# Optimization experiments

Hardware: AMD Instinct MI355X
Metric: run time of the kernel (lower is better)

Reference implementation:

```python
import jax, jax.numpy as jnp
import numpy as np

B, N, C, H = 4, 8192, 1024, 16
D = C // H

def setup_inputs() -> dict:
    key = jax.random.key(0)
    k1, k2, k3 = jax.random.split(key, 3)
    scale_in = 1.0 / np.sqrt(C)
    return {
        "x": jax.random.normal(k1, (B, N, C), dtype=jnp.float32),
        "w_qkv": jax.random.normal(k2, (C, 3 * C), dtype=jnp.float32) * scale_in,
        "b_qkv": jnp.zeros((3 * C,), dtype=jnp.float32),
        "w_proj": jax.random.normal(k3, (C, C), dtype=jnp.float32) * scale_in,
        "b_proj": jnp.zeros((C,), dtype=jnp.float32),
    }

def reference(x, w_qkv, b_qkv, w_proj, b_proj):
    Bx, Nx, Cx = x.shape
    qkv = x @ w_qkv + b_qkv                       # [B,N,3C]
    qkv = qkv.reshape(Bx, Nx, 3, H, D)
    qkv = jnp.transpose(qkv, (2, 0, 3, 1, 4))     # [3,B,H,N,D]
    q, k, v = qkv[0], qkv[1], qkv[2]
    q = jax.nn.elu(q) + 1.0                       # positive feature map
    k = jax.nn.elu(k) + 1.0
    kv = jnp.einsum('bhnd,bhne->bhde', k, v)      # [B,H,D,D]
    out = jnp.einsum('bhnd,bhde->bhne', q, kv)    # [B,H,N,D]
    z = 1.0 / (jnp.einsum('bhnd,bhd->bhn', q, k.sum(axis=2)) + 1e-8)
    out = out * z[..., None]
    out = jnp.transpose(out, (0, 2, 1, 3)).reshape(Bx, Nx, Cx)
    out = out @ w_proj + b_proj                   # dropout is identity in eval
    return out
```

## Files before the change

kernel.cpp:

```cpp
#include <hip/hip_runtime.h>
#include <hip/hip_bf16.h>
#include <stdint.h>

typedef unsigned short ushort_t;
typedef __attribute__((ext_vector_type(8))) short short8;
typedef __attribute__((ext_vector_type(4))) short short4v;
typedef __attribute__((ext_vector_type(4))) float floatx4;

__device__ __forceinline__ ushort_t f2b(float f) {
    unsigned u = __float_as_uint(f);
    unsigned r = (u + 0x7FFFu + ((u >> 16) & 1u)) >> 16;
    return (ushort_t)r;
}
__device__ __forceinline__ float b2f(ushort_t h) {
    return __uint_as_float(((unsigned)h) << 16);
}
__device__ __forceinline__ float elu1(float f) {
    return (f > 0.f) ? (f + 1.f) : __expf(f);
}

#define GLDS16(srcp, dstp)                                                          \
    __builtin_amdgcn_global_load_lds(                                               \
        (const __attribute__((address_space(1))) unsigned int*)(srcp),              \
        (__attribute__((address_space(3))) unsigned int*)(dstp), 16, 0, 0)

__device__ __forceinline__ short4v tr16(const ushort_t* p) {
    short4v r;
    const __attribute__((address_space(3))) ushort_t* p3 =
        (const __attribute__((address_space(3))) ushort_t*)p;
    asm volatile("ds_read_b64_tr_b16 %0, %1" : "=v"(r) : "v"(p3));
    return r;
}


__global__ void conv_bf16(const float* __restrict__ in, ushort_t* __restrict__ out, int n8) {
    for (int i = blockIdx.x * blockDim.x + threadIdx.x; i < n8; i += gridDim.x * blockDim.x) {
        const float4 f0 = *(const float4*)&in[(size_t)i * 8];
        const float4 f1 = *(const float4*)&in[(size_t)i * 8 + 4];
        ushort4 o0, o1;
        o0.x = f2b(f0.x); o0.y = f2b(f0.y); o0.z = f2b(f0.z); o0.w = f2b(f0.w);
        o1.x = f2b(f1.x); o1.y = f2b(f1.y); o1.z = f2b(f1.z); o1.w = f2b(f1.w);
        *(ushort4*)&out[(size_t)i * 8]     = o0;
        *(ushort4*)&out[(size_t)i * 8 + 4] = o1;
    }
}

__global__ void transpose_conv(const float* __restrict__ in, ushort_t* __restrict__ out,
                               int R, int C) {
    __shared__ float tile[32][33];
    int c0 = blockIdx.x * 32, r0 = blockIdx.y * 32;
    int tx = threadIdx.x, ty = threadIdx.y;
#pragma unroll
    for (int k = 0; k < 4; ++k) {
        int a = ty * 4 + k;
        tile[a][tx] = in[(size_t)(r0 + a) * C + c0 + tx];
    }
    __syncthreads();
#pragma unroll
    for (int k = 0; k < 4; ++k) {
        int a = ty * 4 + k;
        out[(size_t)(c0 + a) * R + r0 + tx] = f2b(tile[tx][a]);
    }
}

__global__ void zero_f32(float* __restrict__ p, int n) {
    int i = blockIdx.x * blockDim.x + threadIdx.x;
    if (i < n) p[i] = 0.f;
}

template<int MODE>
__global__ __launch_bounds__(512, 2) void gemm256(
    const ushort_t* __restrict__ A, const ushort_t* __restrict__ Bt,
    const float* __restrict__ bias,
    ushort_t* __restrict__ out_u16, float* __restrict__ out_f32,
    int Nt, int nbx, int nt)
{
    extern __shared__ ushort_t lds[];
    constexpr int KK = 1024;

    const int tid  = threadIdx.x;
    const int wave = tid >> 6;
    const int lane = tid & 63;
    const int wm_i = wave >> 2;
    const int wn_i = wave & 3;
    const int fr   = lane & 15;
    const int fq   = lane >> 4;

    const int bid  = (int)blockIdx.x;
    const int bswz = ((bid & 7) << 5) + (bid >> 3);
    const int ntiles = nt << 8;

    const int trow = tid >> 3;
    const int csw  = ((tid & 7) ^ (trow & 7)) << 3;
    const int tcolB = ((tid >> 8) << 6) + (trow & 31);

    const int dstA = wave * 512;
    const int dstB = 16384 + wave * 512;

    const int sw0 = (fq ^ (fr & 7)) << 3;
    const int sw1 = sw0 ^ 32;
    const int abase = (wm_i * 64 + fr) * 64;
    const int bbase = (wn_i * 32 + fr) * 64;
    int loA0[2][2], loA1[2][2], loB0[2][2], loB1[2][2];
#pragma unroll
    for (int bf = 0; bf < 2; ++bf)
#pragma unroll
        for (int q = 0; q < 2; ++q) {
            loA0[bf][q] = bf * 32768 + q * 8192 + abase + sw0;
            loA1[bf][q] = bf * 32768 + q * 8192 + abase + sw1;
            loB0[bf][q] = bf * 32768 + 16384 + q * 8192 + bbase + sw0;
            loB1[bf][q] = bf * 32768 + 16384 + q * 8192 + bbase + sw1;
        }

    floatx4 acc[8][4];
    const floatx4 z4 = {0.f, 0.f, 0.f, 0.f};
#pragma unroll
    for (int i = 0; i < 8; ++i)
#pragma unroll
        for (int j = 0; j < 4; ++j) acc[i][j] = z4;

    short8 a[4][2], b[2][2];

    auto tilebase = [&](int t, const ushort_t*& sA, const ushort_t*& sB, int& mm, int& nn) {
        const int byy = t / nbx;
        const int bxx = t - byy * nbx;
        mm = byy << 8; nn = bxx << 8;
        sA = A  + (size_t)(mm + trow)  * KK + csw;
        sB = Bt + (size_t)(nn + tcolB) * KK + csw;
    };

    auto stageA = [&](const ushort_t* sp, int buf, int h, int ko) {
        ushort_t* d = lds + buf * 32768 + h * 8192 + dstA;
        GLDS16(sp + h * (64 * KK) + ko, d);
        GLDS16(sp + h * (64 * KK) + 128 * KK + ko, d + 4096);
    };
    auto stageB = [&](const ushort_t* sp, int buf, int h, int ko) {
        ushort_t* d = lds + buf * 32768 + h * 8192 + dstB;
        GLDS16(sp + h * (32 * KK) + ko, d);
        GLDS16(sp + h * (32 * KK) + 128 * KK + ko, d + 4096);
    };
    auto loadA = [&](int buf, int qr) {
        const int o0 = loA0[buf][qr], o1 = loA1[buf][qr];
#pragma unroll
        for (int i = 0; i < 4; ++i) {
            a[i][0] = *(const short8*)(lds + o0 + i * 1024);
            a[i][1] = *(const short8*)(lds + o1 + i * 1024);
        }
    };
    auto loadB = [&](int buf, int qc) {
        const int o0 = loB0[buf][qc], o1 = loB1[buf][qc];
#pragma unroll
        for (int j = 0; j < 2; ++j) {
            b[j][0] = *(const short8*)(lds + o0 + j * 1024);
            b[j][1] = *(const short8*)(lds + o1 + j * 1024);
        }
    };
    auto mma = [&](int qr, int qc) {
#pragma unroll
        for (int i = 0; i < 4; ++i)
#pragma unroll
            for (int j = 0; j < 2; ++j) {
                acc[qr * 4 + i][qc * 2 + j] =
                    __builtin_amdgcn_mfma_f32_16x16x32_bf16(b[j][0], a[i][0], acc[qr * 4 + i][qc * 2 + j], 0, 0, 0);
                acc[qr * 4 + i][qc * 2 + j] =
                    __builtin_amdgcn_mfma_f32_16x16x32_bf16(b[j][1], a[i][1], acc[qr * 4 + i][qc * 2 + j], 0, 0, 0);
            }
    };

    auto epilogue = [&](int m0, int n0) {
        float4 bv[4];
#pragma unroll
        for (int cj = 0; cj < 4; ++cj) {
            const int nb = n0 + wn_i * 64 + (cj >> 1) * 32 + (cj & 1) * 16 + fq * 4;
            bv[cj] = *(const float4*)&bias[nb];
        }
#pragma unroll
        for (int ri = 0; ri < 8; ++ri) {
            const int m = m0 + wm_i * 128 + (ri >> 2) * 64 + (ri & 3) * 16 + fr;
#pragma unroll
            for (int cj = 0; cj < 4; ++cj) {
                const int col = n0 + wn_i * 64 + (cj >> 1) * 32 + (cj & 1) * 16 + fq * 4;
                float v0 = acc[ri][cj][0] + bv[cj].x;
                float v1 = acc[ri][cj][1] + bv[cj].y;
                float v2 = acc[ri][cj][2] + bv[cj].z;
                float v3 = acc[ri][cj][3] + bv[cj].w;
                if (MODE == 0) {
                    const int s  = col >> 10;
                    const int c  = col & 1023;
                    const int h  = c >> 6;
                    const int d  = c & 63;
                    const int bb = m >> 13;
                    const int n  = m & 8191;
                    if (s < 2) { v0 = elu1(v0); v1 = elu1(v1); v2 = elu1(v2); v3 = elu1(v3); }
                    ushort4 o;
                    o.x = f2b(v0); o.y = f2b(v1); o.z = f2b(v2); o.w = f2b(v3);
                    *(ushort4*)&out_u16[(((size_t)s * 64 + bb * 16 + h) * 8192 + n) * 64 + d] = o;
                } else {
                    float4 o; o.x = v0; o.y = v1; o.z = v2; o.w = v3;
                    *(float4*)&out_f32[(size_t)m * Nt + col] = o;
                }
            }
        }
    };

#define PRIO1() __builtin_amdgcn_s_setprio(1)
#define BOUT()  __builtin_amdgcn_s_setprio(0); __builtin_amdgcn_s_barrier()
#define VM6()   asm volatile("s_waitcnt vmcnt(6)" ::: "memory")

    const ushort_t *saC, *sbC, *saN, *sbN;
    int m0, n0, m0N, n0N;
    int tC = bswz;
    tilebase(tC, saC, sbC, m0, n0);
    int tN = (tC + 256 < ntiles) ? tC + 256 : tC;
    tilebase(tN, saN, sbN, m0N, n0N);

    stageA(saC, 0, 0, 0);
    stageB(sbC, 0, 1, 0);
    stageA(saC, 0, 1, 0);
    stageB(sbC, 0, 0, 0);
    stageA(saC, 1, 0, 64);
    stageB(sbC, 1, 1, 64);
    stageA(saC, 1, 1, 64);
    VM6();
    __builtin_amdgcn_s_barrier();

    for (int ot = 0; ot < nt; ++ot) {
        int ko = 0;
        for (int pr = 0; pr < 7; ++pr, ko += 128) {
            loadA(0, 0); loadB(0, 0);
            stageB(sbC, 1, 0, ko + 64);
            PRIO1(); mma(0, 0); BOUT();

            loadB(0, 1);
            stageA(saC, 0, 0, ko + 128);
            PRIO1(); mma(0, 1); BOUT();

            loadA(0, 1);
            stageB(sbC, 0, 1, ko + 128);
            PRIO1(); mma(1, 1); BOUT();

            loadB(0, 0);
            stageA(saC, 0, 1, ko + 128);
            PRIO1(); mma(1, 0); __builtin_amdgcn_s_setprio(0); VM6();
            __builtin_amdgcn_s_barrier();

            loadA(1, 0); loadB(1, 0);
            stageB(sbC, 0, 0, ko + 128);
            PRIO1(); mma(0, 0); BOUT();

            loadB(1, 1);
            stageA(saC, 1, 0, ko + 192);
            PRIO1(); mma(0, 1); BOUT();

            loadA(1, 1);
            stageB(sbC, 1, 1, ko + 192);
            PRIO1(); mma(1, 1); BOUT();

            loadB(1, 0);
            stageA(saC, 1, 1, ko + 192);
            PRIO1(); mma(1, 0); __builtin_amdgcn_s_setprio(0); VM6();
            __builtin_amdgcn_s_barrier();
        }

        loadA(0, 0); loadB(0, 0);
        stageB(sbC, 1, 0, 960);
        PRIO1(); mma(0, 0); BOUT();

        loadB(0, 1);
        stageA(saN, 0, 0, 0);
        PRIO1(); mma(0, 1); BOUT();

        loadA(0, 1);
        stageB(sbN, 0, 1, 0);
        PRIO1(); mma(1, 1); BOUT();

        loadB(0, 0);
        stageA(saN, 0, 1, 0);
        PRIO1(); mma(1, 0); __builtin_amdgcn_s_setprio(0); VM6();
        __builtin_amdgcn_s_barrier();

        loadA(1, 0); loadB(1, 0);
        stageB(sbN, 0, 0, 0);
        PRIO1(); mma(0, 0); BOUT();

        loadB(1, 1);
        stageA(saN, 1, 0, 64);
        PRIO1(); mma(0, 1); BOUT();

        loadA(1, 1);
        stageB(sbN, 1, 1, 64);
        PRIO1(); mma(1, 1); BOUT();

        loadB(1, 0);
        stageA(saN, 1, 1, 64);
        PRIO1(); mma(1, 0); __builtin_amdgcn_s_setprio(0); VM6();
        __builtin_amdgcn_s_barrier();

        epilogue(m0, n0);
#pragma unroll
        for (int i = 0; i < 8; ++i)
#pragma unroll
            for (int j = 0; j < 4; ++j) acc[i][j] = z4;

        saC = saN; sbC = sbN; m0 = m0N; n0 = n0N; tC = tN;
        tN = (tC + 256 < ntiles) ? tC + 256 : tC;
        tilebase(tN, saN, sbN, m0N, n0N);
    }

#undef PRIO1
#undef BOUT
#undef VM6
}

__global__ __launch_bounds__(256) void kvg2_kernel(
    const ushort_t* __restrict__ kbuf, const ushort_t* __restrict__ vbuf,
    float* __restrict__ kv, float* __restrict__ ksum)
{
    __shared__ ushort_t stg[4][2][4096] __attribute__((aligned(16)));
    __shared__ float ksr[4][64];

    const int bh = blockIdx.y, chunk = blockIdx.x, t = threadIdx.x;
    const int wave = t >> 6, lane = t & 63;
    const int fr = lane & 15, fq = lane >> 4;

    const int srow = lane >> 3;
    const int dcp  = lane & 7;
    const int woff = (dcp >> 1) * 1024 + srow * 16 + (dcp & 1) * 8;

    const int troff = fq * 256 + fr * 8;

    short8 ones;
#pragma unroll
    for (int i = 0; i < 8; ++i) ones[i] = (short)0x3F80;

    floatx4 av[4][4], ak[4];
    const floatx4 z4 = {0.f, 0.f, 0.f, 0.f};
#pragma unroll
    for (int i = 0; i < 4; ++i) {
        ak[i] = z4;
#pragma unroll
        for (int j = 0; j < 4; ++j) av[i][j] = z4;
    }

    const size_t rowbase = (size_t)bh * 8192;
    ushort_t* kreg = &stg[wave][0][0];
    ushort_t* vreg = &stg[wave][1][0];

#pragma unroll 1
    for (int s2 = 0; s2 < 4; ++s2) {
        const int n0 = chunk * 1024 + wave * 256 + s2 * 64;
#pragma unroll
        for (int g = 0; g < 8; ++g) {
            const int n = g * 8 + srow;
            const size_t src = (rowbase + n0 + n) * 64 + dcp * 8;
            *(short8*)&kreg[woff + g * 128] = *(const short8*)&kbuf[src];
            *(short8*)&vreg[woff + g * 128] = *(const short8*)&vbuf[src];
        }
        asm volatile("s_waitcnt lgkmcnt(0)" ::: "memory");
        __builtin_amdgcn_sched_barrier(0);

#pragma unroll
        for (int ns = 0; ns < 2; ++ns) {
            short8 ka[4], vb[4];
#pragma unroll
            for (int dt = 0; dt < 4; ++dt) {
                const ushort_t* kb = kreg + dt * 1024 + ns * 512;
                short4v lo = tr16((const ushort_t*)((const char*)kb + troff));
                short4v hi = tr16((const ushort_t*)((const char*)kb + troff + 128));
                ka[dt] = __builtin_shufflevector(lo, hi, 0, 1, 2, 3, 4, 5, 6, 7);
            }
#pragma unroll
            for (int et = 0; et < 4; ++et) {
                const ushort_t* vB = vreg + et * 1024 + ns * 512;
                short4v lo = tr16((const ushort_t*)((const char*)vB + troff));
                short4v hi = tr16((const ushort_t*)((const char*)vB + troff + 128));
                vb[et] = __builtin_shufflevector(lo, hi, 0, 1, 2, 3, 4, 5, 6, 7);
            }
            asm volatile("s_waitcnt lgkmcnt(0)" ::: "memory");
            __builtin_amdgcn_sched_barrier(0);

#pragma unroll
            for (int dt = 0; dt < 4; ++dt) {
                ak[dt] = __builtin_amdgcn_mfma_f32_16x16x32_bf16(ka[dt], ones, ak[dt], 0, 0, 0);
#pragma unroll
                for (int et = 0; et < 4; ++et)
                    av[dt][et] = __builtin_amdgcn_mfma_f32_16x16x32_bf16(ka[dt], vb[et], av[dt][et], 0, 0, 0);
            }
        }
    }

    float* red = (float*)&stg[wave][0][0];
#pragma unroll
    for (int dt = 0; dt < 4; ++dt)
#pragma unroll
        for (int et = 0; et < 4; ++et)
#pragma unroll
            for (int r = 0; r < 4; ++r)
                red[(dt * 16 + fq * 4 + r) * 64 + et * 16 + fr] = av[dt][et][r];
    if (fr == 0) {
#pragma unroll
        for (int dt = 0; dt < 4; ++dt)
#pragma unroll
            for (int r = 0; r < 4; ++r)
                ksr[wave][dt * 16 + fq * 4 + r] = ak[dt][r];
    }
    __syncthreads();

    const float* base = (const float*)&stg[0][0][0];
#pragma unroll
    for (int j = 0; j < 4; ++j) {
        const int idx = t * 16 + j * 4;
        float4 s0 = *(const float4*)&base[0 * 4096 + idx];
        float4 s1 = *(const float4*)&base[1 * 4096 + idx];
        float4 s2 = *(const float4*)&base[2 * 4096 + idx];
        float4 s3 = *(const float4*)&base[3 * 4096 + idx];
        atomicAdd(&kv[(size_t)bh * 4096 + idx + 0], s0.x + s1.x + s2.x + s3.x);
        atomicAdd(&kv[(size_t)bh * 4096 + idx + 1], s0.y + s1.y + s2.y + s3.y);
        atomicAdd(&kv[(size_t)bh * 4096 + idx + 2], s0.z + s1.z + s2.z + s3.z);
        atomicAdd(&kv[(size_t)bh * 4096 + idx + 3], s0.w + s1.w + s2.w + s3.w);
    }
    if (t < 64) {
        float s = ksr[0][t] + ksr[1][t] + ksr[2][t] + ksr[3][t];
        atomicAdd(&ksum[bh * 64 + t], s);
    }
}

__global__ __launch_bounds__(256) void out_kernel(
    const ushort_t* __restrict__ qbuf, const float* __restrict__ kv,
    const float* __restrict__ ksum, ushort_t* __restrict__ obuf)
{
    __shared__ float kvs[4096];
    __shared__ float ksums[64];

    const int bh = blockIdx.y, chunk = blockIdx.x, t = threadIdx.x;
    const int b = bh >> 4, h = bh & 15;
    const int wave = t >> 6, lane = t & 63;
    const int tok = lane & 15, fq = lane >> 4;

#pragma unroll
    for (int i = 0; i < 4; ++i) {
        int idx = (i * 256 + t) * 4;
        *(float4*)&kvs[idx] = *(const float4*)&kv[(size_t)bh * 4096 + idx];
    }
    if (t < 64) ksums[t] = ksum[bh * 64 + t];
    __syncthreads();

    short8 afr[4][2];
#pragma unroll
    for (int et = 0; et < 4; ++et)
#pragma unroll
        for (int kslice = 0; kslice < 2; ++kslice)
#pragma unroll
            for (int i = 0; i < 8; ++i) {
                const int d = kslice * 32 + fq * 8 + i;
                afr[et][kslice][i] = (short)f2b(kvs[d * 64 + et * 16 + tok]);
            }
    short8 zfr[2];
#pragma unroll
    for (int kslice = 0; kslice < 2; ++kslice)
#pragma unroll
        for (int i = 0; i < 8; ++i)
            zfr[kslice][i] = (short)f2b(ksums[kslice * 32 + fq * 8 + i]);

    const floatx4 z4 = {0.f, 0.f, 0.f, 0.f};
    const int nbase = chunk * 1024 + wave * 256;
    const ushort_t* qrow = qbuf + ((size_t)bh * 8192 + nbase + tok) * 64 + fq * 8;
    ushort_t* orow = obuf + ((size_t)b * 8192 + nbase + tok) * 1024 + h * 64 + fq * 4;

#pragma unroll 2
    for (int g = 0; g < 16; ++g) {
        short8 bf0 = *(const short8*)(qrow + (size_t)g * 16 * 64);
        short8 bf1 = *(const short8*)(qrow + (size_t)g * 16 * 64 + 32);

        floatx4 az = __builtin_amdgcn_mfma_f32_16x16x32_bf16(zfr[0], bf0, z4, 0, 0, 0);
        az = __builtin_amdgcn_mfma_f32_16x16x32_bf16(zfr[1], bf1, az, 0, 0, 0);

        floatx4 ad[4];
#pragma unroll
        for (int et = 0; et < 4; ++et) {
            ad[et] = __builtin_amdgcn_mfma_f32_16x16x32_bf16(afr[et][0], bf0, z4, 0, 0, 0);
            ad[et] = __builtin_amdgcn_mfma_f32_16x16x32_bf16(afr[et][1], bf1, ad[et], 0, 0, 0);
        }

        const float zi = 1.f / (az[0] + 1e-8f);
#pragma unroll
        for (int et = 0; et < 4; ++et) {
            ushort4 o;
            o.x = f2b(ad[et][0] * zi);
            o.y = f2b(ad[et][1] * zi);
            o.z = f2b(ad[et][2] * zi);
            o.w = f2b(ad[et][3] * zi);
            *(ushort4*)&orow[(size_t)g * 16 * 1024 + et * 16] = o;
        }
    }
}


extern "C" void kernel_launch(void* const* d_in, const int* in_sizes, int n_in,
                              void* d_out, int out_size, void* d_ws, size_t ws_size,
                              hipStream_t stream) {
    const float* x      = (const float*)d_in[0];
    const float* w_qkv  = (const float*)d_in[1];
    const float* b_qkv  = (const float*)d_in[2];
    const float* w_proj = (const float*)d_in[3];
    const float* b_proj = (const float*)d_in[4];
    float* out = (float*)d_out;

    const size_t XE = (size_t)32768 * 1024;

    char* ws = (char*)d_ws;
    ushort_t* xb   = (ushort_t*)ws;  ws += XE * 2;
    ushort_t* wqT  = (ushort_t*)ws;  ws += (size_t)3072 * 1024 * 2;
    ushort_t* wpT  = (ushort_t*)ws;  ws += (size_t)1024 * 1024 * 2;
    ushort_t* qkvb = (ushort_t*)ws;  ws += 3 * XE * 2;
    ushort_t* ob   = (ushort_t*)ws;  ws += XE * 2;
    float*    kv   = (float*)ws;     ws += (size_t)64 * 64 * 64 * 4;
    float*    ksum = (float*)ws;     ws += (size_t)64 * 64 * 4;

    (void)hipFuncSetAttribute(reinterpret_cast<const void*>(gemm256<0>),
                              hipFuncAttributeMaxDynamicSharedMemorySize, 131072);
    (void)hipFuncSetAttribute(reinterpret_cast<const void*>(gemm256<1>),
                              hipFuncAttributeMaxDynamicSharedMemorySize, 131072);

    zero_f32<<<dim3((64 * 64 * 64 + 64 * 64 + 255) / 256), dim3(256), 0, stream>>>(kv, 64 * 64 * 64 + 64 * 64);
    conv_bf16<<<dim3(2048), dim3(256), 0, stream>>>(x, xb, (int)(XE / 8));
    transpose_conv<<<dim3(96, 32), dim3(32, 8), 0, stream>>>(w_qkv, wqT, 1024, 3072);
    transpose_conv<<<dim3(32, 32), dim3(32, 8), 0, stream>>>(w_proj, wpT, 1024, 1024);

    gemm256<0><<<dim3(256), dim3(512), 131072, stream>>>(xb, wqT, b_qkv, qkvb, nullptr, 3072, 12, 6);

    kvg2_kernel<<<dim3(8, 64), dim3(256), 0, stream>>>(qkvb + XE, qkvb + 2 * XE, kv, ksum);
    out_kernel<<<dim3(8, 64), dim3(256), 0, stream>>>(qkvb, kv, ksum, ob);

    gemm256<1><<<dim3(256), dim3(512), 131072, stream>>>(ob, wpT, b_proj, nullptr, out, 1024, 4, 2);
}
```

Baseline: 486.9 us.

## Store K and V in MFMA-ready layout from QKV GEMM epilogue, drop LDS transpose

After: 488.5 us. About the same (+0.3%).

```diff
diff --git a/kernel.cpp b/kernel.cpp
--- a/kernel.cpp
+++ b/kernel.cpp
@@ -4,7 +4,6 @@
 
 typedef unsigned short ushort_t;
 typedef __attribute__((ext_vector_type(8))) short short8;
-typedef __attribute__((ext_vector_type(4))) short short4v;
 typedef __attribute__((ext_vector_type(4))) float floatx4;
 
 __device__ __forceinline__ ushort_t f2b(float f) {
@@ -23,14 +22,6 @@
     __builtin_amdgcn_global_load_lds(                                               \
         (const __attribute__((address_space(1))) unsigned int*)(srcp),              \
         (__attribute__((address_space(3))) unsigned int*)(dstp), 16, 0, 0)
-
-__device__ __forceinline__ short4v tr16(const ushort_t* p) {
-    short4v r;
-    const __attribute__((address_space(3))) ushort_t* p3 =
-        (const __attribute__((address_space(3))) ushort_t*)p;
-    asm volatile("ds_read_b64_tr_b16 %0, %1" : "=v"(r) : "v"(p3));
-    return r;
-}
 
 
 __global__ void conv_bf16(const float* __restrict__ in, ushort_t* __restrict__ out, int n8) {
@@ -77,6 +68,7 @@
 {
     extern __shared__ ushort_t lds[];
     constexpr int KK = 1024;
+    constexpr size_t XEc = (size_t)32768 * 1024;
 
     const int tid  = threadIdx.x;
     const int wave = tid >> 6;
@@ -191,10 +183,21 @@
                     const int d  = c & 63;
                     const int bb = m >> 13;
                     const int n  = m & 8191;
-                    if (s < 2) { v0 = elu1(v0); v1 = elu1(v1); v2 = elu1(v2); v3 = elu1(v3); }
-                    ushort4 o;
-                    o.x = f2b(v0); o.y = f2b(v1); o.z = f2b(v2); o.w = f2b(v3);
-                    *(ushort4*)&out_u16[(((size_t)s * 64 + bb * 16 + h) * 8192 + n) * 64 + d] = o;
+                    const int bh = bb * 16 + h;
+                    if (s == 0) {
+                        v0 = elu1(v0); v1 = elu1(v1); v2 = elu1(v2); v3 = elu1(v3);
+                        ushort4 o;
+                        o.x = f2b(v0); o.y = f2b(v1); o.z = f2b(v2); o.w = f2b(v3);
+                        *(ushort4*)&out_u16[((size_t)bh * 8192 + n) * 64 + d] = o;
+                    } else {
+                        if (s == 1) { v0 = elu1(v0); v1 = elu1(v1); v2 = elu1(v2); v3 = elu1(v3); }
+                        ushort_t* dst = out_u16 + ((s == 1) ? XEc : 2 * XEc);
+                        const size_t base = ((size_t)(bh * 1024 + (n >> 3)) * 64 + d) * 8 + (n & 7);
+                        dst[base]      = f2b(v0);
+                        dst[base + 8]  = f2b(v1);
+                        dst[base + 16] = f2b(v2);
+                        dst[base + 24] = f2b(v3);
+                    }
                 } else {
                     float4 o; o.x = v0; o.y = v1; o.z = v2; o.w = v3;
                     *(float4*)&out_f32[(size_t)m * Nt + col] = o;
@@ -312,23 +315,17 @@
 #undef VM6
 }
 
-__global__ __launch_bounds__(256) void kvg2_kernel(
-    const ushort_t* __restrict__ kbuf, const ushort_t* __restrict__ vbuf,
+__global__ __launch_bounds__(256) void kvg3_kernel(
+    const ushort_t* __restrict__ kb, const ushort_t* __restrict__ vb,
     float* __restrict__ kv, float* __restrict__ ksum)
 {
-    __shared__ ushort_t stg[4][2][4096] __attribute__((aligned(16)));
+    __shared__ float red[4][4096];
     __shared__ float ksr[4][64];
 
     const int bh = blockIdx.y, chunk = blockIdx.x, t = threadIdx.x;
     const int wave = t >> 6, lane = t & 63;
     const int fr = lane & 15, fq = lane >> 4;
 
-    const int srow = lane >> 3;
-    const int dcp  = lane & 7;
-    const int woff = (dcp >> 1) * 1024 + srow * 16 + (dcp & 1) * 8;
-
-    const int troff = fq * 256 + fr * 8;
-
     short8 ones;
 #pragma unroll
     for (int i = 0; i < 8; ++i) ones[i] = (short)0x3F80;
@@ -342,61 +339,35 @@
         for (int j = 0; j < 4; ++j) av[i][j] = z4;
     }
 
-    const size_t rowbase = (size_t)bh * 8192;
-    ushort_t* kreg = &stg[wave][0][0];
-    ushort_t* vreg = &stg[wave][1][0];
-
-#pragma unroll 1
-    for (int s2 = 0; s2 < 4; ++s2) {
-        const int n0 = chunk * 1024 + wave * 256 + s2 * 64;
-#pragma unroll
-        for (int g = 0; g < 8; ++g) {
-            const int n = g * 8 + srow;
-            const size_t src = (rowbase + n0 + n) * 64 + dcp * 8;
-            *(short8*)&kreg[woff + g * 128] = *(const short8*)&kbuf[src];
-            *(short8*)&vreg[woff + g * 128] = *(const short8*)&vbuf[src];
-        }
-        asm volatile("s_waitcnt lgkmcnt(0)" ::: "memory");
-        __builtin_amdgcn_sched_barrier(0);
-
-#pragma unroll
-        for (int ns = 0; ns < 2; ++ns) {
-            short8 ka[4], vb[4];
-#pragma unroll
-            for (int dt = 0; dt < 4; ++dt) {
-                const ushort_t* kb = kreg + dt * 1024 + ns * 512;
-                short4v lo = tr16((const ushort_t*)((const char*)kb + troff));
-                short4v hi = tr16((const ushort_t*)((const char*)kb + troff + 128));
-                ka[dt] = __builtin_shufflevector(lo, hi, 0, 1, 2, 3, 4, 5, 6, 7);
-            }
-#pragma unroll
-            for (int et = 0; et < 4; ++et) {
-                const ushort_t* vB = vreg + et * 1024 + ns * 512;
-                short4v lo = tr16((const ushort_t*)((const char*)vB + troff));
-                short4v hi = tr16((const ushort_t*)((const char*)vB + troff + 128));
-                vb[et] = __builtin_shufflevector(lo, hi, 0, 1, 2, 3, 4, 5, 6, 7);
-            }
-            asm volatile("s_waitcnt lgkmcnt(0)" ::: "memory");
-            __builtin_amdgcn_sched_barrier(0);
-
-#pragma unroll
-            for (int dt = 0; dt < 4; ++dt) {
-                ak[dt] = __builtin_amdgcn_mfma_f32_16x16x32_bf16(ka[dt], ones, ak[dt], 0, 0, 0);
-#pragma unroll
-                for (int et = 0; et < 4; ++et)
-                    av[dt][et] = __builtin_amdgcn_mfma_f32_16x16x32_bf16(ka[dt], vb[et], av[dt][et], 0, 0, 0);
-            }
-        }
-    }
-
-    float* red = (float*)&stg[wave][0][0];
+    const size_t base = ((size_t)bh * 1024 + chunk * 128 + wave * 32 + fq) * 512 + fr * 8;
+    const ushort_t* kp = kb + base;
+    const ushort_t* vp = vb + base;
+
+#pragma unroll 2
+    for (int s = 0; s < 8; ++s) {
+        short8 ka[4], va[4];
+#pragma unroll
+        for (int dt = 0; dt < 4; ++dt)
+            ka[dt] = *(const short8*)(kp + s * 2048 + dt * 128);
+#pragma unroll
+        for (int et = 0; et < 4; ++et)
+            va[et] = *(const short8*)(vp + s * 2048 + et * 128);
+#pragma unroll
+        for (int dt = 0; dt < 4; ++dt) {
+            ak[dt] = __builtin_amdgcn_mfma_f32_16x16x32_bf16(ka[dt], ones, ak[dt], 0, 0, 0);
+#pragma unroll
+            for (int et = 0; et < 4; ++et)
+                av[dt][et] = __builtin_amdgcn_mfma_f32_16x16x32_bf16(ka[dt], va[et], av[dt][et], 0, 0, 0);
+        }
+    }
+
 #pragma unroll
     for (int dt = 0; dt < 4; ++dt)
 #pragma unroll
         for (int et = 0; et < 4; ++et)
 #pragma unroll
             for (int r = 0; r < 4; ++r)
-                red[(dt * 16 + fq * 4 + r) * 64 + et * 16 + fr] = av[dt][et][r];
+                red[wave][(dt * 16 + fq * 4 + r) * 64 + et * 16 + fr] = av[dt][et][r];
     if (fr == 0) {
 #pragma unroll
         for (int dt = 0; dt < 4; ++dt)
@@ -406,14 +377,13 @@
     }
     __syncthreads();
 
-    const float* base = (const float*)&stg[0][0][0];
 #pragma unroll
     for (int j = 0; j < 4; ++j) {
         const int idx = t * 16 + j * 4;
-        float4 s0 = *(const float4*)&base[0 * 4096 + idx];
-        float4 s1 = *(const float4*)&base[1 * 4096 + idx];
-        float4 s2 = *(const float4*)&base[2 * 4096 + idx];
-        float4 s3 = *(const float4*)&base[3 * 4096 + idx];
+        float4 s0 = *(const float4*)&red[0][idx];
+        float4 s1 = *(const float4*)&red[1][idx];
+        float4 s2 = *(const float4*)&red[2][idx];
+        float4 s3 = *(const float4*)&red[3][idx];
         atomicAdd(&kv[(size_t)bh * 4096 + idx + 0], s0.x + s1.x + s2.x + s3.x);
         atomicAdd(&kv[(size_t)bh * 4096 + idx + 1], s0.y + s1.y + s2.y + s3.y);
         atomicAdd(&kv[(size_t)bh * 4096 + idx + 2], s0.z + s1.z + s2.z + s3.z);
@@ -529,7 +499,7 @@
 
     gemm256<0><<<dim3(256), dim3(512), 131072, stream>>>(xb, wqT, b_qkv, qkvb, nullptr, 3072, 12, 6);
 
-    kvg2_kernel<<<dim3(8, 64), dim3(256), 0, stream>>>(qkvb + XE, qkvb + 2 * XE, kv, ksum);
+    kvg3_kernel<<<dim3(8, 64), dim3(256), 0, stream>>>(qkvb + XE, qkvb + 2 * XE, kv, ksum);
     out_kernel<<<dim3(8, 64), dim3(256), 0, stream>>>(qkvb, kv, ksum, ob);
 
     gemm256<1><<<dim3(256), dim3(512), 131072, stream>>>(ob, wpT, b_proj, nullptr, out, 1024, 4, 2);
```
